# Kernel tuning notes

Measured on AMD Instinct MI355X. Metric: run time of the kernel, lower is better.

## Reference

```python
import jax, jax.numpy as jnp
import numpy as np

D_MODEL = 1024
NUM_HEADS = 16
D_K = D_MODEL // NUM_HEADS  # 64
THETA = 10000.0
B, S = 2, 2048


def _rope(x, cos, sin):
    # x: [b, h, s, d]; cos/sin: [s, d//2] (broadcast over b, h)
    x1 = x[..., 0::2]
    x2 = x[..., 1::2]
    y1 = x1 * cos - x2 * sin
    y2 = x1 * sin + x2 * cos
    # interleave back: stack on last dim then flatten pairs
    return jnp.stack([y1, y2], axis=-1).reshape(x.shape)


def setup_inputs() -> dict:
    key = jax.random.key(0)
    ks = jax.random.split(key, 5)
    scale = 1.0 / np.sqrt(D_MODEL)
    return {
        "x": jax.random.normal(ks[0], (B, S, D_MODEL), dtype=jnp.float32),
        "token_positions": jnp.arange(S, dtype=jnp.int32),
        "Wq": jax.random.normal(ks[1], (D_MODEL, D_MODEL), dtype=jnp.float32) * scale,
        "Wk": jax.random.normal(ks[2], (D_MODEL, D_MODEL), dtype=jnp.float32) * scale,
        "Wv": jax.random.normal(ks[3], (D_MODEL, D_MODEL), dtype=jnp.float32) * scale,
        "Wo": jax.random.normal(ks[4], (D_MODEL, D_MODEL), dtype=jnp.float32) * scale,
    }


def reference(x, token_positions, Wq, Wk, Wv, Wo):
    b, s, _ = x.shape
    # torch nn.Linear semantics (no bias in this repo's Linear): y = x @ W.T
    q = jnp.einsum("bsd,od->bso", x, Wq)
    k = jnp.einsum("bsd,od->bso", x, Wk)
    v = jnp.einsum("bsd,od->bso", x, Wv)
    # split heads: b s (h d) -> b h s d
    def split(t):
        return t.reshape(b, s, NUM_HEADS, D_K).transpose(0, 2, 1, 3)
    q, k, v = split(q), split(k), split(v)

    # RoPE tables
    inv_freq = 1.0 / (THETA ** (jnp.arange(0, D_K, 2, dtype=jnp.float32) / D_K))  # [d/2]
    freqs = token_positions.astype(jnp.float32)[:, None] * inv_freq[None, :]      # [s, d/2]
    cos, sin = jnp.cos(freqs), jnp.sin(freqs)
    q = _rope(q, cos, sin)
    k = _rope(k, cos, sin)

    scale = D_K ** (-0.5)
    scores = jnp.einsum("bhqd,bhkd->bhqk", q, k) * scale  # [b,h,s,s]
    causal = jnp.tril(jnp.ones((s, s), dtype=bool))
    scores = jnp.where(causal, scores, -jnp.inf)
    attn = jax.nn.softmax(scores, axis=-1)
    out = jnp.einsum("bhqk,bhkd->bhqd", attn, v)
    out = out.transpose(0, 2, 1, 3).reshape(b, s, D_MODEL)  # b h s d -> b s (h d)
    return jnp.einsum("bsd,od->bso", out, Wo)
```

## Files before the change

kernel.cpp:

```cpp
#include <hip/hip_runtime.h>
#include <hip/hip_bf16.h>
#include <math.h>

#define SS 2048

typedef __attribute__((ext_vector_type(8))) __bf16 bf16x8;
typedef __attribute__((ext_vector_type(4))) float f32x4;
typedef __attribute__((ext_vector_type(16))) float f32x16;
typedef __attribute__((ext_vector_type(4))) unsigned int u32x4;
typedef __attribute__((ext_vector_type(4))) unsigned short u16x4;

__device__ __forceinline__ f32x4 mfma16(bf16x8 a, bf16x8 b, f32x4 c) {
  return __builtin_amdgcn_mfma_f32_16x16x32_bf16(a, b, c, 0, 0, 0);
}
__device__ __forceinline__ f32x16 mfma32(bf16x8 a, bf16x8 b, f32x16 c) {
  return __builtin_amdgcn_mfma_f32_32x32x16_bf16(a, b, c, 0, 0, 0);
}

__device__ __forceinline__ void gld_lds16(const void* g, void* l) {
  __builtin_amdgcn_global_load_lds(
      (__attribute__((address_space(1))) void*)(g),
      (__attribute__((address_space(3))) void*)(l), 16, 0, 0);
}

#if __has_builtin(__builtin_amdgcn_exp2f)
#define EXP2F(x) __builtin_amdgcn_exp2f(x)
#else
#define EXP2F(x) __expf(0.69314718056f * (x))
#endif

__device__ __forceinline__ unsigned int cvtpk_bf16(float lo, float hi) {
  unsigned int r;
  asm("v_cvt_pk_bf16_f32 %0, %1, %2" : "=v"(r) : "v"(lo), "v"(hi));
  return r;
}
__device__ __forceinline__ void swap32(unsigned int& x, unsigned int& y) {
  asm("v_permlane32_swap_b32 %0, %1" : "+v"(x), "+v"(y));
}
__device__ __forceinline__ unsigned short bfu(float v) {
  __bf16 h = (__bf16)v;
  return __builtin_bit_cast(unsigned short, h);
}

__global__ void prep_kernel(const float* __restrict__ x, const float* __restrict__ Wq,
                            const float* __restrict__ Wk, const float* __restrict__ Wv,
                            const float* __restrict__ Wo, const int* __restrict__ pos,
                            __bf16* __restrict__ xb, __bf16* __restrict__ Wb,
                            float2* __restrict__ tab) {
  const int bid = blockIdx.x, tid = threadIdx.x;
  if (bid >= 4096) {
    int i = (bid - 4096) * 256 + tid;
    int s = i >> 5, j = i & 31;
    float p = (float)pos[s];
    float inv = exp2f((float)j * -0.41524101186098283f);
    float f = p * inv;
    float sn, cs;
    sincosf(f, &sn, &cs);
    tab[i] = make_float2(cs, sn);
    return;
  }
  const float* s;
  __bf16* d;
  size_t base;
  if (bid < 2048) { s = x; d = xb; base = bid; }
  else {
    int seg = (bid - 2048) >> 9;
    s = (seg == 0) ? Wq : (seg == 1) ? Wk : (seg == 2) ? Wv : Wo;
    d = Wb + (size_t)seg * 1024 * 1024;
    base = (bid - 2048) & 511;
  }
  size_t i = (base * 256 + tid) * 8;
  float4 a = *reinterpret_cast<const float4*>(s + i);
  float4 b = *reinterpret_cast<const float4*>(s + i + 4);
  bf16x8 o;
  o[0] = (__bf16)a.x; o[1] = (__bf16)a.y; o[2] = (__bf16)a.z; o[3] = (__bf16)a.w;
  o[4] = (__bf16)b.x; o[5] = (__bf16)b.y; o[6] = (__bf16)b.z; o[7] = (__bf16)b.w;
  *reinterpret_cast<bf16x8*>(d + i) = o;
}

template <typename OutT, int MODE>
__global__ __launch_bounds__(512) void gemm128_kernel(
    const __bf16* __restrict__ A, const __bf16* __restrict__ Bw,
    OutT* __restrict__ C, __bf16* __restrict__ Vt,
    int N, const float2* __restrict__ tab) {
  const int K = 1024, nk = 16;
  __shared__ __align__(16) __bf16 sm[32768];
  __bf16* lsA = sm;
  __bf16* lsB = sm + 16384;

  const int tid = threadIdx.x;
  const int lane = tid & 63;
  const int wave = tid >> 6;
  const int wr = wave >> 2, wc = wave & 3;

  const int xcd = blockIdx.x & 7;
  const int ii = blockIdx.x >> 3;
  const int m0 = (4 * xcd + (ii & 3)) * 128;
  const int n0 = (ii >> 2) * 128;

  const f32x4 fzero = {0.f, 0.f, 0.f, 0.f};
  f32x4 acc[4][2];
#pragma unroll
  for (int f = 0; f < 4; ++f)
#pragma unroll
    for (int g = 0; g < 2; ++g) acc[f][g] = fzero;

  const int srow = tid >> 3, sch = tid & 7;
  const int ssc = 8 * (sch ^ (srow & 7));
  const __bf16* gA = A + (size_t)(m0 + srow) * K + ssc;
  const __bf16* gB = Bw + (size_t)(n0 + srow) * K + ssc;
  const size_t h64 = (size_t)64 * K;

#define STAGEG(sl_, kt_)                                              \
  do {                                                                \
    const int ko_ = (kt_) * 64;                                       \
    gld_lds16(gA + ko_, lsA + (sl_) * 8192 + tid * 8);                \
    gld_lds16(gA + h64 + ko_, lsA + (sl_) * 8192 + 4096 + tid * 8);   \
    gld_lds16(gB + ko_, lsB + (sl_) * 8192 + tid * 8);                \
    gld_lds16(gB + h64 + ko_, lsB + (sl_) * 8192 + 4096 + tid * 8);   \
  } while (0)

  STAGEG(0, 0);

  const int lrow = lane & 15, hi = lane >> 4;

#pragma unroll 1
  for (int kt = 0; kt < nk; ++kt) {
    const int buf = kt & 1;
    if (kt + 1 < nk) {
      STAGEG(buf ^ 1, kt + 1);
      asm volatile("s_waitcnt vmcnt(4)" ::: "memory");
    } else {
      asm volatile("s_waitcnt vmcnt(0)" ::: "memory");
    }
    __builtin_amdgcn_s_barrier();

    const __bf16* sA = lsA + buf * 8192;
    const __bf16* sB = lsB + buf * 8192;
    bf16x8 af[4][2], bfr[2][2];
#pragma unroll
    for (int g = 0; g < 2; ++g) {
      const int r = wc * 32 + g * 16 + lrow;
#pragma unroll
      for (int kk = 0; kk < 2; ++kk) {
        const int pc = ((kk << 2) | hi) ^ (r & 7);
        bfr[g][kk] = *reinterpret_cast<const bf16x8*>(sB + r * 64 + pc * 8);
      }
    }
#pragma unroll
    for (int f = 0; f < 4; ++f) {
      const int r = wr * 64 + f * 16 + lrow;
#pragma unroll
      for (int kk = 0; kk < 2; ++kk) {
        const int pc = ((kk << 2) | hi) ^ (r & 7);
        af[f][kk] = *reinterpret_cast<const bf16x8*>(sA + r * 64 + pc * 8);
      }
    }
    __builtin_amdgcn_s_setprio(1);
#pragma unroll
    for (int f = 0; f < 4; ++f)
#pragma unroll
      for (int g = 0; g < 2; ++g) {
        acc[f][g] = mfma16(af[f][0], bfr[g][0], acc[f][g]);
        acc[f][g] = mfma16(af[f][1], bfr[g][1], acc[f][g]);
      }
    __builtin_amdgcn_s_setprio(0);
    __builtin_amdgcn_s_barrier();
  }
#undef STAGEG

  const int crow = (lane >> 4) * 4, ccol = lane & 15;
  if (MODE == 1) {
    const int par = ccol & 1;
#pragma unroll
    for (int g = 0; g < 2; ++g) {
      const int cb = n0 + wc * 32 + g * 16;
      if (cb < 2048) {
        const int jj = ((cb + ccol) >> 1) & 31;
#pragma unroll
        for (int f = 0; f < 4; ++f) {
#pragma unroll
          for (int t = 0; t < 4; ++t) {
            const int r = m0 + wr * 64 + f * 16 + crow + t;
            const int s = r & (SS - 1);
            float2 cs = tab[(s << 5) | jj];
            float v = acc[f][g][t];
            float o = __shfl_xor(v, 1);
            float y = par ? fmaf(o, cs.y, v * cs.x) : fmaf(v, cs.x, -o * cs.y);
            C[(size_t)r * N + cb + ccol] = (OutT)y;
          }
        }
      } else {
        const int c = cb - 2048 + ccol;
        const int hh = c >> 6, dd = c & 63;
#pragma unroll
        for (int f = 0; f < 4; ++f) {
          const int r0 = m0 + wr * 64 + f * 16 + crow;
          const int bb = r0 >> 11, s0 = r0 & (SS - 1);
          u16x4 pk;
#pragma unroll
          for (int t = 0; t < 4; ++t) pk[t] = bfu(acc[f][g][t]);
          *reinterpret_cast<u16x4*>(Vt + ((size_t)(bb * 16 + hh) * 64 + dd) * SS + s0) = pk;
        }
      }
    }
  } else {
#pragma unroll
    for (int f = 0; f < 4; ++f) {
#pragma unroll
      for (int g = 0; g < 2; ++g) {
        int r = m0 + wr * 64 + f * 16 + crow;
        int c = n0 + wc * 32 + g * 16 + ccol;
#pragma unroll
        for (int t = 0; t < 4; ++t) C[(size_t)(r + t) * N + c] = (OutT)acc[f][g][t];
      }
    }
  }
}

#define CEXP 0.18033688011112042f
#define SHIFT_B 16.0f

__device__ __forceinline__ void attn_round(const __bf16* lk, const __bf16* lv,
                                           const bf16x8 (&qb)[4], f32x16& o0,
                                           f32x16& o1, float& lsum, int q,
                                           int kvb, bool diag, int q32, int hi) {
  const f32x16 fz16 = {0,0,0,0,0,0,0,0,0,0,0,0,0,0,0,0};
  f32x16 s0 = fz16, s1 = fz16;
  __builtin_amdgcn_s_setprio(1);
#pragma unroll
  for (int slot = 0; slot < 4; ++slot) {
    const int swz = 8 * ((slot * 2 + hi) ^ (q32 & 7));
    bf16x8 kf0 = *reinterpret_cast<const bf16x8*>(lk + q32 * 64 + swz);
    bf16x8 kf1 = *reinterpret_cast<const bf16x8*>(lk + (32 + q32) * 64 + swz);
    s0 = mfma32(kf0, qb[slot], s0);
    s1 = mfma32(kf1, qb[slot], s1);
  }
  __builtin_amdgcn_s_setprio(0);

  if (diag) {
#pragma unroll
    for (int r = 0; r < 16; ++r) {
      const int rowc = (r & 3) + 8 * (r >> 2) + 4 * hi;
      if (kvb + rowc > q) s0[r] = -INFINITY;
      if (kvb + 32 + rowc > q) s1[r] = -INFINITY;
    }
  }

  {
    float a0 = 0.f, a1 = 0.f, a2 = 0.f, a3 = 0.f;
#pragma unroll
    for (int r = 0; r < 16; r += 4) {
      s0[r] = EXP2F(fmaf(s0[r], CEXP, -SHIFT_B)); a0 += s0[r];
      s0[r + 1] = EXP2F(fmaf(s0[r + 1], CEXP, -SHIFT_B)); a1 += s0[r + 1];
      s0[r + 2] = EXP2F(fmaf(s0[r + 2], CEXP, -SHIFT_B)); a2 += s0[r + 2];
      s0[r + 3] = EXP2F(fmaf(s0[r + 3], CEXP, -SHIFT_B)); a3 += s0[r + 3];
    }
#pragma unroll
    for (int r = 0; r < 16; r += 4) {
      s1[r] = EXP2F(fmaf(s1[r], CEXP, -SHIFT_B)); a0 += s1[r];
      s1[r + 1] = EXP2F(fmaf(s1[r + 1], CEXP, -SHIFT_B)); a1 += s1[r + 1];
      s1[r + 2] = EXP2F(fmaf(s1[r + 2], CEXP, -SHIFT_B)); a2 += s1[r + 2];
      s1[r + 3] = EXP2F(fmaf(s1[r + 3], CEXP, -SHIFT_B)); a3 += s1[r + 3];
    }
    float rs = (a0 + a1) + (a2 + a3);
    rs += __shfl_xor(rs, 32);
    lsum += rs;
  }

  bf16x8 pb[4];
  {
    unsigned int A = cvtpk_bf16(s0[0], s0[1]), B2 = cvtpk_bf16(s0[2], s0[3]);
    unsigned int C2 = cvtpk_bf16(s0[4], s0[5]), D2 = cvtpk_bf16(s0[6], s0[7]);
    swap32(A, C2); swap32(B2, D2);
    u32x4 t0 = {A, B2, C2, D2};
    pb[0] = __builtin_bit_cast(bf16x8, t0);
    unsigned int E = cvtpk_bf16(s0[8], s0[9]), F = cvtpk_bf16(s0[10], s0[11]);
    unsigned int G = cvtpk_bf16(s0[12], s0[13]), H = cvtpk_bf16(s0[14], s0[15]);
    swap32(E, G); swap32(F, H);
    u32x4 t1 = {E, F, G, H};
    pb[1] = __builtin_bit_cast(bf16x8, t1);
    unsigned int A3 = cvtpk_bf16(s1[0], s1[1]), B3 = cvtpk_bf16(s1[2], s1[3]);
    unsigned int C3 = cvtpk_bf16(s1[4], s1[5]), D3 = cvtpk_bf16(s1[6], s1[7]);
    swap32(A3, C3); swap32(B3, D3);
    u32x4 t2 = {A3, B3, C3, D3};
    pb[2] = __builtin_bit_cast(bf16x8, t2);
    unsigned int E3 = cvtpk_bf16(s1[8], s1[9]), F3 = cvtpk_bf16(s1[10], s1[11]);
    unsigned int G3 = cvtpk_bf16(s1[12], s1[13]), H3 = cvtpk_bf16(s1[14], s1[15]);
    swap32(E3, G3); swap32(F3, H3);
    u32x4 t3 = {E3, F3, G3, H3};
    pb[3] = __builtin_bit_cast(bf16x8, t3);
  }

  __builtin_amdgcn_s_setprio(1);
#pragma unroll
  for (int slot = 0; slot < 4; ++slot) {
    const int swz = 8 * ((slot * 2 + hi) ^ (q32 & 7));
    bf16x8 v0 = *reinterpret_cast<const bf16x8*>(lv + q32 * 64 + swz);
    bf16x8 v1 = *reinterpret_cast<const bf16x8*>(lv + (32 + q32) * 64 + swz);
    o0 = mfma32(v0, pb[slot], o0);
    o1 = mfma32(v1, pb[slot], o1);
  }
  __builtin_amdgcn_s_setprio(0);
}

__global__ __launch_bounds__(128) void attn_pair_kernel(
    const __bf16* __restrict__ qkv, const __bf16* __restrict__ Vt,
    __bf16* __restrict__ AO, __bf16* __restrict__ pB, float* __restrict__ pL) {
  const int bid = blockIdx.x;
  const int x = bid & 7, t7 = bid >> 3;
  const int phi = t7 & 3, pi = (t7 >> 2) & 15, half = t7 >> 6;
  const int hp = phi * 8 + x;
  const int b = hp >> 4, h = hp & 15;
  const int qtA = pi, qtB = 31 - pi;
  const int nr = half ? 16 : 17;
  const int segA = half ? 0 : (pi + 1);

  const int tid = threadIdx.x;
  const int wave = tid >> 6, lane = tid & 63;
  const int q32 = lane & 31, hi = lane >> 5;
  const int qA = qtA * 64 + wave * 32 + q32;
  const int qB = qtB * 64 + wave * 32 + q32;

  __shared__ __align__(16) __bf16 smem[16384];

  bf16x8 qbA[4], qbB[4];
  {
    const __bf16* qrA = qkv + (size_t)(b * SS + qA) * 3072 + h * 64;
    const __bf16* qrB = qkv + (size_t)(b * SS + qB) * 3072 + h * 64;
#pragma unroll
    for (int slot = 0; slot < 4; ++slot) {
      qbA[slot] = *reinterpret_cast<const bf16x8*>(qrA + slot * 16 + hi * 8);
      qbB[slot] = *reinterpret_cast<const bf16x8*>(qrB + slot * 16 + hi * 8);
    }
  }
  asm volatile("s_waitcnt vmcnt(0)" ::: "memory");

  const __bf16* kbase = qkv + (size_t)(b * SS) * 3072 + 1024 + h * 64;
  const __bf16* vbase = Vt + (size_t)((b * 16 + h) * 64) * SS;

  const int srow = tid >> 3, scg = tid & 7;
  const int ssc = 8 * (scg ^ (srow & 7));
  const __bf16* kG0 = kbase + (size_t)srow * 3072 + ssc;
  const __bf16* vG0 = vbase + (size_t)srow * SS + ssc;

#define KVOF(r_) (half ? (16 - pi + (r_)) : (((r_) < segA) ? (r_) : ((r_)-segA)))

#define STAGE(buf_, kv_)                                                      \
  do {                                                                        \
    const __bf16* kG = kG0 + (size_t)(kv_)*64 * 3072;                         \
    const __bf16* vG = vG0 + (size_t)(kv_)*64;                                \
    __bf16* sl_ = smem + (buf_)*8192;                                         \
    _Pragma("unroll") for (int u = 0; u < 4; ++u) {                           \
      gld_lds16(kG + (size_t)u * 16 * 3072, sl_ + tid * 8 + u * 1024);        \
      gld_lds16(vG + (size_t)u * 16 * SS, sl_ + 4096 + tid * 8 + u * 1024);   \
    }                                                                         \
  } while (0)

  const f32x16 fz16 = {0,0,0,0,0,0,0,0,0,0,0,0,0,0,0,0};
  f32x16 oA0 = fz16, oA1 = fz16, oB0 = fz16, oB1 = fz16;
  float lA = 0.f, lB = 0.f;

  STAGE(0, KVOF(0));

#pragma unroll 1
  for (int r = 0; r < nr; ++r) {
    const int buf = r & 1;
    if (r + 1 < nr) {
      STAGE(buf ^ 1, KVOF(r + 1));
      asm volatile("s_waitcnt vmcnt(8)" ::: "memory");
    } else {
      asm volatile("s_waitcnt vmcnt(0)" ::: "memory");
    }
    __builtin_amdgcn_s_barrier();

    const __bf16* lk = smem + buf * 8192;
    const __bf16* lv = lk + 4096;
    const int kv = KVOF(r);

    if (r < segA) {
      attn_round(lk, lv, qbA, oA0, oA1, lA, qA, kv * 64, kv == qtA, q32, hi);
    } else {
      attn_round(lk, lv, qbB, oB0, oB1, lB, qB, kv * 64, kv == qtB, q32, hi);
    }

    __builtin_amdgcn_s_barrier();
  }
#undef STAGE
#undef KVOF

  asm volatile("s_waitcnt vmcnt(0)" ::: "memory");
  __builtin_amdgcn_s_barrier();

  __bf16* ol = smem + wave * 2304;
  if (half == 0) {
    const float invA = 1.0f / lA;
#pragma unroll
    for (int r = 0; r < 16; ++r) {
      const int d = (r & 3) + 8 * (r >> 2) + 4 * hi;
      ol[q32 * 72 + d] = (__bf16)(oA0[r] * invA);
      ol[q32 * 72 + 32 + d] = (__bf16)(oA1[r] * invA);
    }
#pragma unroll
    for (int pass = 0; pass < 4; ++pass) {
      const int idx = pass * 64 + lane;
      const int row = idx >> 3, colc = idx & 7;
      bf16x8 v = *reinterpret_cast<const bf16x8*>(ol + row * 72 + colc * 8);
      *reinterpret_cast<bf16x8*>(
          AO + (size_t)(b * SS + qtA * 64 + wave * 32 + row) * 1024 + h * 64 + colc * 8) = v;
    }
#pragma unroll
    for (int r = 0; r < 16; ++r) {
      const int d = (r & 3) + 8 * (r >> 2) + 4 * hi;
      ol[q32 * 72 + d] = (__bf16)oB0[r];
      ol[q32 * 72 + 32 + d] = (__bf16)oB1[r];
    }
#pragma unroll
    for (int pass = 0; pass < 4; ++pass) {
      const int idx = pass * 64 + lane;
      const int row = idx >> 3, colc = idx & 7;
      bf16x8 v = *reinterpret_cast<const bf16x8*>(ol + row * 72 + colc * 8);
      *reinterpret_cast<bf16x8*>(
          AO + (size_t)(b * SS + qtB * 64 + wave * 32 + row) * 1024 + h * 64 + colc * 8) = v;
    }
    if (hi == 0) pL[hp * 2048 + qtB * 64 + wave * 32 + q32] = lB;
  } else {
#pragma unroll
    for (int r = 0; r < 16; ++r) {
      const int d = (r & 3) + 8 * (r >> 2) + 4 * hi;
      ol[q32 * 72 + d] = (__bf16)oB0[r];
      ol[q32 * 72 + 32 + d] = (__bf16)oB1[r];
    }
#pragma unroll
    for (int pass = 0; pass < 4; ++pass) {
      const int idx = pass * 64 + lane;
      const int row = idx >> 3, colc = idx & 7;
      bf16x8 v = *reinterpret_cast<const bf16x8*>(ol + row * 72 + colc * 8);
      *reinterpret_cast<bf16x8*>(
          pB + (size_t)(b * SS + qtB * 64 + wave * 32 + row) * 1024 + h * 64 + colc * 8) = v;
    }
    if (hi == 0) pL[65536 + hp * 2048 + qtB * 64 + wave * 32 + q32] = lB;
  }
}

__global__ void combine_kernel(const __bf16* __restrict__ pB,
                               const float* __restrict__ pL,
                               __bf16* __restrict__ ao) {
  const int e = (blockIdx.x * 256 + threadIdx.x) * 8;
  const int subrow = e >> 10, col = e & 1023;
  const int bb = subrow >> 10, s = 1024 + (subrow & 1023);
  const int h = col >> 6;
  const int bh = bb * 16 + h;
  const size_t i = ((size_t)bb * SS + s) * 1024 + col;
  const float la = pL[bh * 2048 + s];
  const float lb = pL[65536 + bh * 2048 + s];
  const float inv = 1.0f / (la + lb);
  bf16x8 a = *reinterpret_cast<const bf16x8*>(ao + i);
  bf16x8 b8 = *reinterpret_cast<const bf16x8*>(pB + i);
  bf16x8 o;
#pragma unroll
  for (int j = 0; j < 8; ++j) o[j] = (__bf16)(((float)a[j] + (float)b8[j]) * inv);
  *reinterpret_cast<bf16x8*>(ao + i) = o;
}

extern "C" void kernel_launch(void* const* d_in, const int* in_sizes, int n_in,
                              void* d_out, int out_size, void* d_ws, size_t ws_size,
                              hipStream_t stream) {
  const float* x  = (const float*)d_in[0];
  const int* pos  = (const int*)d_in[1];
  const float* Wq = (const float*)d_in[2];
  const float* Wk = (const float*)d_in[3];
  const float* Wv = (const float*)d_in[4];
  const float* Wo = (const float*)d_in[5];

  __bf16* xb  = (__bf16*)d_ws;
  __bf16* Wb  = xb + (size_t)4096 * 1024;
  __bf16* qkv = Wb + (size_t)4096 * 1024;
  __bf16* Vt  = qkv + (size_t)4096 * 3072;
  __bf16* ao  = Vt + (size_t)2048 * 2048;
  float2* tab = (float2*)(ao + (size_t)4096 * 1024);
  __bf16* pB  = (__bf16*)(tab + 2048 * 32);
  float*  pL  = (float*)(pB + (size_t)4096 * 1024);

  prep_kernel<<<4352, 256, 0, stream>>>(x, Wq, Wk, Wv, Wo, pos, xb, Wb, tab);
  gemm128_kernel<__bf16, 1><<<768, 512, 0, stream>>>(xb, Wb, qkv, Vt, 3072, tab);
  attn_pair_kernel<<<1024, 128, 0, stream>>>(qkv, Vt, ao, pB, pL);
  combine_kernel<<<1024, 256, 0, stream>>>(pB, pL, ao);
  gemm128_kernel<float, 0><<<256, 512, 0, stream>>>(
      ao, Wb + (size_t)3 * 1024 * 1024, (float*)d_out, nullptr, 1024, nullptr);
}
```

Measured before the change: 101.7 us.

## Use 256x256 tiled 8-phase pipelined GEMM for the QKV projection

Replaces the 128x128-tile QKV projection GEMM with a 256x256-tile kernel using a four-slot LDS ring and eight barrier-separated phases that interleave fragment loads, async global-to-LDS staging and MFMA. Larger tiles raise operand reuse per block and the phased schedule aims to overlap memory with compute. The trade-off is only 192 blocks for 256 CUs, so some CUs sit idle, plus heavy register and LDS use at one block per CU. The output GEMM is split into its own non-templated kernel.

```diff
diff --git a/kernel.cpp b/kernel.cpp
--- a/kernel.cpp
+++ b/kernel.cpp
@@ -78,12 +78,169 @@
   *reinterpret_cast<bf16x8*>(d + i) = o;
 }
 
-template <typename OutT, int MODE>
-__global__ __launch_bounds__(512) void gemm128_kernel(
+__global__ __launch_bounds__(512, 1) void gemm256_8ph_kernel(
     const __bf16* __restrict__ A, const __bf16* __restrict__ Bw,
-    OutT* __restrict__ C, __bf16* __restrict__ Vt,
-    int N, const float2* __restrict__ tab) {
-  const int K = 1024, nk = 16;
+    __bf16* __restrict__ C, __bf16* __restrict__ Vt,
+    const float2* __restrict__ tab) {
+  const int K = 1024, N = 3072, nk = 16;
+  __shared__ __align__(16) __bf16 sm[65536];
+  __bf16* lsA = sm;
+  __bf16* lsB = sm + 32768;
+
+  const int tid = threadIdx.x;
+  const int lane = tid & 63;
+  const int wave = tid >> 6;
+  const int wr = wave >> 2, wc = wave & 3, wch = wc >> 1;
+
+  const int xcd = blockIdx.x & 7;
+  const int ii = blockIdx.x >> 3;
+  const int m0 = (2 * xcd + (ii & 1)) * 256;
+  const int n0 = (ii >> 1) * 256;
+
+  const f32x4 fzero = {0.f, 0.f, 0.f, 0.f};
+  f32x4 acc[8][4];
+#pragma unroll
+  for (int f = 0; f < 8; ++f)
+#pragma unroll
+    for (int g = 0; g < 4; ++g) acc[f][g] = fzero;
+
+  const __bf16* gAu[4];
+  const __bf16* gBu[4];
+  int dAo[4], dBo[4];
+  {
+    const int sgB = (wr << 1) | (wc & 1);
+#pragma unroll
+    for (int u = 0; u < 4; ++u) {
+      int ciA = wc * 256 + u * 64 + lane;
+      int rA = ciA >> 3, cA = ciA & 7;
+      gAu[u] = A + (size_t)(m0 + wr * 128 + rA) * K + 8 * (cA ^ (rA & 7));
+      dAo[u] = ciA * 8;
+      int ciB = sgB * 256 + u * 64 + lane;
+      int rB = ciB >> 3, cB = ciB & 7;
+      gBu[u] = Bw + (size_t)(n0 + wch * 128 + rB) * K + 8 * (cB ^ (rB & 7));
+      dBo[u] = ciB * 8;
+    }
+  }
+
+#define STAGE_A(kt_)                                                          \
+  {                                                                           \
+    const int sl_ = (2 * (kt_) + wr) & 3;                                     \
+    _Pragma("unroll") for (int u = 0; u < 4; ++u)                             \
+        gld_lds16(gAu[u] + (kt_)*64, lsA + sl_ * 8192 + dAo[u]);              \
+  }
+#define STAGE_B(kt_)                                                          \
+  {                                                                           \
+    const int sl_ = (2 * (kt_) + wch) & 3;                                    \
+    _Pragma("unroll") for (int u = 0; u < 4; ++u)                             \
+        gld_lds16(gBu[u] + (kt_)*64, lsB + sl_ * 8192 + dBo[u]);              \
+  }
+
+  const int lrow = lane & 15, hi = lane >> 4;
+
+  bf16x8 af[4][2], bf0[2][2], bf1[2][2];
+
+#define LDA(BASE, F0)                                                         \
+  _Pragma("unroll") for (int j = 0; j < 4; ++j) {                             \
+    const int rr = ((F0) + j) * 16 + lrow;                                    \
+    _Pragma("unroll") for (int kk = 0; kk < 2; ++kk) {                        \
+      const int pc = ((kk << 2) | hi) ^ (rr & 7);                             \
+      af[j][kk] = *reinterpret_cast<const bf16x8*>((BASE) + rr * 64 + pc * 8);\
+    }                                                                         \
+  }
+#define LDB(DST, BASE, G0)                                                    \
+  _Pragma("unroll") for (int j = 0; j < 2; ++j) {                             \
+    const int rb = (wc & 1) * 64 + ((G0) + j) * 16 + lrow;                    \
+    _Pragma("unroll") for (int kk = 0; kk < 2; ++kk) {                        \
+      const int pc = ((kk << 2) | hi) ^ (rb & 7);                             \
+      DST[j][kk] = *reinterpret_cast<const bf16x8*>((BASE) + rb * 64 + pc * 8);\
+    }                                                                         \
+  }
+#define MM(F0, G0, BF)                                                        \
+  __builtin_amdgcn_s_setprio(1);                                              \
+  _Pragma("unroll") for (int j = 0; j < 4; ++j) {                             \
+    _Pragma("unroll") for (int g2 = 0; g2 < 2; ++g2) {                        \
+      acc[(F0) + j][(G0) + g2] = mfma16(af[j][0], BF[g2][0], acc[(F0) + j][(G0) + g2]); \
+      acc[(F0) + j][(G0) + g2] = mfma16(af[j][1], BF[g2][1], acc[(F0) + j][(G0) + g2]); \
+    }                                                                         \
+  }                                                                           \
+  __builtin_amdgcn_s_setprio(0);
+
+  STAGE_A(0);
+  STAGE_B(0);
+  asm volatile("s_waitcnt vmcnt(0)" ::: "memory");
+  __builtin_amdgcn_s_barrier();
+
+#pragma unroll 1
+  for (int kt = 0; kt < nk; ++kt) {
+    const __bf16* bA = lsA + (size_t)(((2 * kt + wr) & 3)) * 8192;
+    const __bf16* bB = lsB + (size_t)(((2 * kt + wch) & 3)) * 8192;
+    LDA(bA, 0)
+    LDB(bf0, bB, 0)
+    if (kt + 1 < nk) STAGE_A(kt + 1)
+    __builtin_amdgcn_s_barrier();
+    MM(0, 0, bf0)
+    __builtin_amdgcn_s_barrier();
+    LDB(bf1, bB, 2)
+    if (kt + 1 < nk) STAGE_B(kt + 1)
+    __builtin_amdgcn_s_barrier();
+    MM(0, 2, bf1)
+    __builtin_amdgcn_s_barrier();
+    LDA(bA, 4)
+    __builtin_amdgcn_s_barrier();
+    MM(4, 2, bf1)
+    __builtin_amdgcn_s_barrier();
+    LDB(bf0, bB, 0)
+    asm volatile("s_waitcnt vmcnt(0)" ::: "memory");
+    __builtin_amdgcn_s_barrier();
+    MM(4, 0, bf0)
+    __builtin_amdgcn_s_barrier();
+  }
+#undef MM
+#undef LDB
+#undef LDA
+#undef STAGE_B
+#undef STAGE_A
+
+  const int crow = (lane >> 4) * 4, ccol = lane & 15;
+  const int par = ccol & 1;
+#pragma unroll
+  for (int g = 0; g < 4; ++g) {
+    const int cb = n0 + wc * 64 + g * 16;
+    if (cb < 2048) {
+      const int jj = ((cb + ccol) >> 1) & 31;
+#pragma unroll
+      for (int f = 0; f < 8; ++f) {
+#pragma unroll
+        for (int t = 0; t < 4; ++t) {
+          const int r = m0 + wr * 128 + f * 16 + crow + t;
+          const int s = r & (SS - 1);
+          float2 cs = tab[(s << 5) | jj];
+          float v = acc[f][g][t];
+          float o = __shfl_xor(v, 1);
+          float y = par ? fmaf(o, cs.y, v * cs.x) : fmaf(v, cs.x, -o * cs.y);
+          C[(size_t)r * N + cb + ccol] = (__bf16)y;
+        }
+      }
+    } else {
+      const int c = cb - 2048 + ccol;
+      const int hh = c >> 6, dd = c & 63;
+#pragma unroll
+      for (int f = 0; f < 8; ++f) {
+        const int r0 = m0 + wr * 128 + f * 16 + crow;
+        const int bb = r0 >> 11, s0 = r0 & (SS - 1);
+        u16x4 pk;
+#pragma unroll
+        for (int t = 0; t < 4; ++t) pk[t] = bfu(acc[f][g][t]);
+        *reinterpret_cast<u16x4*>(Vt + ((size_t)(bb * 16 + hh) * 64 + dd) * SS + s0) = pk;
+      }
+    }
+  }
+}
+
+__global__ __launch_bounds__(512) void gemm_out_kernel(
+    const __bf16* __restrict__ A, const __bf16* __restrict__ Bw,
+    float* __restrict__ C) {
+  const int K = 1024, N = 1024, nk = 16;
   __shared__ __align__(16) __bf16 sm[32768];
   __bf16* lsA = sm;
   __bf16* lsB = sm + 16384;
@@ -170,50 +327,14 @@
 #undef STAGEG
 
   const int crow = (lane >> 4) * 4, ccol = lane & 15;
-  if (MODE == 1) {
-    const int par = ccol & 1;
+#pragma unroll
+  for (int f = 0; f < 4; ++f) {
 #pragma unroll
     for (int g = 0; g < 2; ++g) {
-      const int cb = n0 + wc * 32 + g * 16;
-      if (cb < 2048) {
-        const int jj = ((cb + ccol) >> 1) & 31;
-#pragma unroll
-        for (int f = 0; f < 4; ++f) {
-#pragma unroll
-          for (int t = 0; t < 4; ++t) {
-            const int r = m0 + wr * 64 + f * 16 + crow + t;
-            const int s = r & (SS - 1);
-            float2 cs = tab[(s << 5) | jj];
-            float v = acc[f][g][t];
-            float o = __shfl_xor(v, 1);
-            float y = par ? fmaf(o, cs.y, v * cs.x) : fmaf(v, cs.x, -o * cs.y);
-            C[(size_t)r * N + cb + ccol] = (OutT)y;
-          }
-        }
-      } else {
-        const int c = cb - 2048 + ccol;
-        const int hh = c >> 6, dd = c & 63;
-#pragma unroll
-        for (int f = 0; f < 4; ++f) {
-          const int r0 = m0 + wr * 64 + f * 16 + crow;
-          const int bb = r0 >> 11, s0 = r0 & (SS - 1);
-          u16x4 pk;
-#pragma unroll
-          for (int t = 0; t < 4; ++t) pk[t] = bfu(acc[f][g][t]);
-          *reinterpret_cast<u16x4*>(Vt + ((size_t)(bb * 16 + hh) * 64 + dd) * SS + s0) = pk;
-        }
-      }
-    }
-  } else {
-#pragma unroll
-    for (int f = 0; f < 4; ++f) {
-#pragma unroll
-      for (int g = 0; g < 2; ++g) {
-        int r = m0 + wr * 64 + f * 16 + crow;
-        int c = n0 + wc * 32 + g * 16 + ccol;
-#pragma unroll
-        for (int t = 0; t < 4; ++t) C[(size_t)(r + t) * N + c] = (OutT)acc[f][g][t];
-      }
+      int r = m0 + wr * 64 + f * 16 + crow;
+      int c = n0 + wc * 32 + g * 16 + ccol;
+#pragma unroll
+      for (int t = 0; t < 4; ++t) C[(size_t)(r + t) * N + c] = acc[f][g][t];
     }
   }
 }
@@ -483,9 +604,8 @@
   float*  pL  = (float*)(pB + (size_t)4096 * 1024);
 
   prep_kernel<<<4352, 256, 0, stream>>>(x, Wq, Wk, Wv, Wo, pos, xb, Wb, tab);
-  gemm128_kernel<__bf16, 1><<<768, 512, 0, stream>>>(xb, Wb, qkv, Vt, 3072, tab);
+  gemm256_8ph_kernel<<<192, 512, 0, stream>>>(xb, Wb, qkv, Vt, tab);
   attn_pair_kernel<<<1024, 128, 0, stream>>>(qkv, Vt, ao, pB, pL);
   combine_kernel<<<1024, 256, 0, stream>>>(pB, pL, ao);
-  gemm128_kernel<float, 0><<<256, 512, 0, stream>>>(
-      ao, Wb + (size_t)3 * 1024 * 1024, (float*)d_out, nullptr, 1024, nullptr);
-}
+  gemm_out_kernel<<<256, 512, 0, stream>>>(ao, Wb + (size_t)3 * 1024 * 1024, (float*)d_out);
+}
```

Result: slower. 105.4 us (+3.6%).
